# Performance work log

Measured on AMD Instinct MI355X. Metric: run time of the kernel, lower is better.

The kernel has to match this reference:

```python
import jax, jax.numpy as jnp
import numpy as np

D_MODEL = 1024
HEADS = 16
HEAD_DIM = D_MODEL // HEADS


def setup_inputs() -> dict:
    key = jax.random.key(0)
    ks = jax.random.split(key, 6)
    B, S, D = 2, 2048, D_MODEL
    scale = 1.0 / np.sqrt(D)
    x = jax.random.normal(ks[0], (B, S, D), dtype=jnp.float32)
    mask = jax.random.randint(ks[1], (B, S), 0, 2, dtype=jnp.int32)
    Wq = jax.random.normal(ks[2], (D, D), dtype=jnp.float32) * scale
    Wk = jax.random.normal(ks[3], (D, D), dtype=jnp.float32) * scale
    Wv = jax.random.normal(ks[4], (D, D), dtype=jnp.float32) * scale
    Wp = jax.random.normal(ks[5], (D, D), dtype=jnp.float32) * scale
    zb = jnp.zeros((D,), dtype=jnp.float32)
    return {"x": x, "mask": mask, "Wq": Wq, "bq": zb, "Wk": Wk, "bk": zb,
            "Wv": Wv, "bv": zb, "Wp": Wp, "bp": zb}


def reference(x, mask, Wq, bq, Wk, bk, Wv, bv, Wp, bp):
    B, S, D = x.shape
    H, Dh = HEADS, HEAD_DIM

    def split_heads(t):  # [B,S,D] -> [B,H,S,Dh]
        return t.reshape(B, S, H, Dh).transpose(0, 2, 1, 3)

    q = split_heads(x @ Wq + bq)
    k = split_heads(x @ Wk + bk)
    v = split_heads(x @ Wv + bv)

    att = jnp.einsum('bhqd,bhkd->bhqk', q, k) / jnp.sqrt(jnp.float32(Dh))
    # key-padding mask: [B,S] -> [B,1,1,S]; masked positions -> -inf
    m = (mask[:, None, None, :] != 0)
    att = jnp.where(m, att, -jnp.inf)
    att = jax.nn.softmax(att, axis=-1)
    # rows that were fully masked produce NaN -> zero them (masked_fill(isnan, 0))
    att = jnp.where(jnp.isnan(att), 0.0, att)

    y = jnp.einsum('bhqk,bhkd->bhqd', att, v)  # [B,H,S,Dh]
    y = y.transpose(0, 2, 1, 3).reshape(B, S, D)
    return y @ Wp + bp
```

## Files before the change

### kernel.cpp

```cpp
#include <hip/hip_runtime.h>
#include <math.h>

#define D_MODEL 1024
#define HEADS 16
#define HEAD_DIM 64
#define SEQ 2048
#define BATCH 2
#define KVT 64
#define QTILE 128
#define SCALE_Q 0.18033688f

typedef __attribute__((ext_vector_type(8))) short bf16x8;
typedef __attribute__((ext_vector_type(4))) float f32x4;

__device__ __forceinline__ short f2bf(float f) {
    union { float f; unsigned u; } v; v.f = f;
    unsigned r = (v.u + 0x7FFFu + ((v.u >> 16) & 1u)) >> 16;
    return (short)r;
}

__device__ __forceinline__ unsigned cvt_pk_bf16(float lo, float hi) {
    unsigned r;
    asm("v_cvt_pk_bf16_f32 %0, %1, %2" : "=v"(r) : "v"(lo), "v"(hi));
    return r;
}

__device__ __forceinline__ float fexp2(float x) {
    float r;
    asm("v_exp_f32 %0, %1" : "=v"(r) : "v"(x));
    return r;
}

__global__ __launch_bounds__(256) void prep(
    const float* __restrict__ x, const float* __restrict__ Wq,
    const float* __restrict__ Wk, const float* __restrict__ Wv,
    const float* __restrict__ Wp, const int* __restrict__ mask,
    short* __restrict__ xb, short* __restrict__ Wqkvt,
    short* __restrict__ Wpt, float* __restrict__ maskf) {
    __shared__ float t[32][33];
    const int bid = blockIdx.x;
    if (bid < 2048) {
        const int i = bid * 256 + threadIdx.x;
        float4 a = ((const float4*)x)[2 * i];
        float4 b = ((const float4*)x)[2 * i + 1];
        short r[8] = {f2bf(a.x), f2bf(a.y), f2bf(a.z), f2bf(a.w),
                      f2bf(b.x), f2bf(b.y), f2bf(b.z), f2bf(b.w)};
        *(uint4*)(xb + 8 * i) = *(uint4*)r;
    } else if (bid < 6144) {
        const int tt = bid - 2048;
        const int z = tt >> 10;
        const int rem = tt & 1023;
        const float* W = z == 0 ? Wq : z == 1 ? Wk : z == 2 ? Wv : Wp;
        short* dst = (z < 3) ? Wqkvt + (size_t)z * 1024 * 1024 : Wpt;
        const int n0 = (rem & 31) * 32, k0 = (rem >> 5) * 32;
        const int tx = threadIdx.x & 31, ty = threadIdx.x >> 5;
#pragma unroll
        for (int j = 0; j < 4; ++j)
            t[ty + j * 8][tx] = W[(size_t)(k0 + ty + j * 8) * 1024 + n0 + tx];
        __syncthreads();
#pragma unroll
        for (int j = 0; j < 4; ++j) {
            const int n = ty + j * 8;
            dst[(size_t)(n0 + n) * 1024 + k0 + tx] = f2bf(t[tx][n]);
        }
    } else {
        const int i = (bid - 6144) * 256 + threadIdx.x;
        maskf[i] = mask[i] ? 0.f : -INFINITY;
    }
}

template <int MODE>
__global__ __launch_bounds__(256) void mfma_gemm(
    const short* __restrict__ A, const short* __restrict__ Bt,
    const float* __restrict__ b0, const float* __restrict__ b1,
    const float* __restrict__ b2, float* __restrict__ outf,
    short* __restrict__ o0, short* __restrict__ o1, short* __restrict__ o2,
    int M, int N, int K) {
    __shared__ short As[2 * 128 * 32];
    __shared__ short Bs[2 * 128 * 32];

    const int tid = threadIdx.x;
    const int wave = tid >> 6, lane = tid & 63;
    const int l15 = lane & 15, lhi = lane >> 4;
    const int wm = wave >> 1, wn = wave & 1;

    const int nwgx = gridDim.x;
    const int nwg = nwgx * gridDim.y;
    const int lin = blockIdx.y * nwgx + blockIdx.x;
    const int swz = (lin & 7) * (nwg >> 3) + (lin >> 3);
    const int bm0 = (swz / nwgx) * 128, bn0 = (swz % nwgx) * 128;

    f32x4 acc[4][4];
#pragma unroll
    for (int m = 0; m < 4; ++m)
#pragma unroll
        for (int n = 0; n < 4; ++n) acc[m][n] = (f32x4){0.f, 0.f, 0.f, 0.f};

#define STAGE_G(buf, kt_)                                                         \
    {                                                                             \
        const int k0 = (kt_) * 32;                                                \
        _Pragma("unroll") for (int p = 0; p < 2; ++p) {                           \
            const int o = (wave * 2 + p) * 64 + lane;                             \
            const int r = o >> 2;                                                 \
            const int gs = (o & 3) ^ ((r >> 1) & 3);                              \
            __builtin_amdgcn_global_load_lds(                                     \
                (const __attribute__((address_space(1))) void*)(                  \
                    A + (size_t)(bm0 + r) * K + k0 + gs * 8),                     \
                (__attribute__((address_space(3))) void*)(                        \
                    As + (size_t)(buf) * 4096 + (wave * 2 + p) * 512),            \
                16, 0, 0);                                                        \
            __builtin_amdgcn_global_load_lds(                                     \
                (const __attribute__((address_space(1))) void*)(                  \
                    Bt + (size_t)(bn0 + r) * K + k0 + gs * 8),                    \
                (__attribute__((address_space(3))) void*)(                        \
                    Bs + (size_t)(buf) * 4096 + (wave * 2 + p) * 512),            \
                16, 0, 0);                                                        \
        }                                                                         \
    }

    const int NT = K / 32;
    STAGE_G(0, 0);
    __syncthreads();
    for (int kt = 0; kt < NT; ++kt) {
        const int cur = kt & 1;
        if (kt + 1 < NT) STAGE_G((kt + 1) & 1, kt + 1);
        bf16x8 af[4], bf[4];
        const int sg = (lhi ^ ((l15 >> 1) & 3)) * 16;
#pragma unroll
        for (int m = 0; m < 4; ++m)
            af[m] = *(const bf16x8*)((char*)As + cur * 8192 +
                                     (wm * 64 + m * 16 + l15) * 64 + sg);
#pragma unroll
        for (int n = 0; n < 4; ++n)
            bf[n] = *(const bf16x8*)((char*)Bs + cur * 8192 +
                                     (wn * 64 + n * 16 + l15) * 64 + sg);
        __builtin_amdgcn_s_setprio(1);
#pragma unroll
        for (int m = 0; m < 4; ++m)
#pragma unroll
            for (int n = 0; n < 4; ++n)
                acc[m][n] = __builtin_amdgcn_mfma_f32_16x16x32_bf16(af[m], bf[n], acc[m][n], 0, 0, 0);
        __builtin_amdgcn_s_setprio(0);
        __syncthreads();
    }
#undef STAGE_G

    const int which = (MODE == 1) ? (bn0 >> 10) : 0;
#pragma unroll
    for (int m = 0; m < 4; ++m) {
#pragma unroll
        for (int n = 0; n < 4; ++n) {
            const int col = bn0 + wn * 64 + n * 16 + l15;
            if (MODE == 0) {
#pragma unroll
                for (int rr = 0; rr < 4; ++rr) {
                    const int row = bm0 + wm * 64 + m * 16 + lhi * 4 + rr;
                    outf[(size_t)row * N + col] = acc[m][n][rr] + b0[col];
                }
            } else {
                const int cc = col & 1023;
                const int h = cc >> 6, dh = cc & 63;
                const int row0 = bm0 + wm * 64 + m * 16 + lhi * 4;
                const int b = row0 >> 11, s0 = row0 & (SEQ - 1);
                if (which == 2) {
                    const float bias = b2[cc];
                    uint2 w;
                    w.x = cvt_pk_bf16(acc[m][n][0] + bias, acc[m][n][1] + bias);
                    w.y = cvt_pk_bf16(acc[m][n][2] + bias, acc[m][n][3] + bias);
                    *(uint2*)(o2 + ((size_t)(b * HEADS + h) * HEAD_DIM + dh) * SEQ + s0) = w;
                } else {
                    const float bias = (which == 0 ? b0 : b1)[cc];
                    short* dst = which == 0 ? o0 : o1;
#pragma unroll
                    for (int rr = 0; rr < 4; ++rr) {
                        float v = acc[m][n][rr] + bias;
                        if (which == 0) v *= SCALE_Q;
                        dst[(((size_t)(b * HEADS + h)) * SEQ + s0 + rr) * HEAD_DIM + dh] = f2bf(v);
                    }
                }
            }
        }
    }
}

__global__ __launch_bounds__(256, 2) void flash_attn(
    const short* __restrict__ Q, const short* __restrict__ K,
    const short* __restrict__ Vt, const float* __restrict__ maskf,
    short* __restrict__ Y) {
    __shared__ unsigned char kt[2][KVT * 128];
    __shared__ unsigned char vt[2][HEAD_DIM * 128];
    __shared__ unsigned char pb[4][32 * 128];

    const int tid = threadIdx.x;
    const int wave = tid >> 6;
    const int lane = tid & 63;
    const int l15 = lane & 15;
    const int lhi = lane >> 4;

    const int nwg = gridDim.x;
    const int wg = blockIdx.x;
    const int swz = (wg & 7) * (nwg >> 3) + (wg >> 3);
    const int qt = swz & 15;
    const int bh = swz >> 4;
    const int b = bh >> 4;

    const int q0 = qt * QTILE + wave * 32;

    bf16x8 qf[2][2];
#pragma unroll
    for (int qi = 0; qi < 2; ++qi) {
        const short* Qp = Q + ((size_t)bh * SEQ + q0 + 16 * qi + l15) * HEAD_DIM;
        qf[qi][0] = *(const bf16x8*)(Qp + 8 * lhi);
        qf[qi][1] = *(const bf16x8*)(Qp + 8 * lhi + 32);
    }

    const unsigned char* Kb8 = (const unsigned char*)(K + (size_t)bh * SEQ * HEAD_DIM);
    const unsigned char* Vb8 = (const unsigned char*)(Vt + (size_t)bh * HEAD_DIM * SEQ);
    const float* mb = maskf + b * SEQ;

#define STAGE(buf, kvi)                                                            \
    {                                                                              \
        const unsigned char* kbase = Kb8 + (size_t)(kvi) * KVT * 128;              \
        const unsigned char* vbase = Vb8 + (size_t)(kvi) * 128;                    \
        _Pragma("unroll") for (int p = 0; p < 2; ++p) {                            \
            const int o = (wave * 2 + p) * 64 + lane;                              \
            const int row = o >> 3;                                                \
            const int inner = (o & 7) * 16;                                        \
            const int src = inner ^ ((row & 7) << 4);                              \
            __builtin_amdgcn_global_load_lds(                                      \
                (const __attribute__((address_space(1))) void*)(                   \
                    kbase + row * 128 + src),                                      \
                (__attribute__((address_space(3))) void*)(                         \
                    &kt[buf][(wave * 2 + p) * 1024]),                              \
                16, 0, 0);                                                         \
            __builtin_amdgcn_global_load_lds(                                      \
                (const __attribute__((address_space(1))) void*)(                   \
                    &vt[buf][0] == nullptr ? nullptr :                             \
                    vbase + (size_t)row * (SEQ * 2) + src),                        \
                (__attribute__((address_space(3))) void*)(                         \
                    &vt[buf][(wave * 2 + p) * 1024]),                              \
                16, 0, 0);                                                         \
        }                                                                          \
    }

    f32x4 accO[2][4];
    float lrow[2] = {0.f, 0.f};
#pragma unroll
    for (int qi = 0; qi < 2; ++qi)
#pragma unroll
        for (int i = 0; i < 4; ++i) accO[qi][i] = (f32x4){0.f, 0.f, 0.f, 0.f};

    STAGE(0, 0);
    asm volatile("s_waitcnt vmcnt(0)" ::: "memory");
    __builtin_amdgcn_s_barrier();

    for (int kv = 0; kv < SEQ / KVT; ++kv) {
        const int cur = kv & 1;
        if (kv + 1 < SEQ / KVT) STAGE((kv + 1) & 1, kv + 1);
        asm volatile("s_waitcnt vmcnt(4)" ::: "memory");
        __builtin_amdgcn_sched_barrier(0);
        __builtin_amdgcn_s_barrier();

        const int k0 = kv * KVT;

        f32x4 accS[2][4];
#pragma unroll
        for (int qi = 0; qi < 2; ++qi)
#pragma unroll
            for (int nt = 0; nt < 4; ++nt) accS[qi][nt] = (f32x4){0.f, 0.f, 0.f, 0.f};
#pragma unroll
        for (int c = 0; c < 2; ++c) {
            bf16x8 kf[4];
#pragma unroll
            for (int nt = 0; nt < 4; ++nt) {
                const int key = l15 + 16 * nt;
                kf[nt] = *(const bf16x8*)(kt[cur] + key * 128 +
                                          ((16 * lhi + 64 * c) ^ ((key & 7) << 4)));
            }
            __builtin_amdgcn_s_setprio(1);
#pragma unroll
            for (int qi = 0; qi < 2; ++qi)
#pragma unroll
                for (int nt = 0; nt < 4; ++nt)
                    accS[qi][nt] = __builtin_amdgcn_mfma_f32_16x16x32_bf16(
                        kf[nt], qf[qi][c], accS[qi][nt], 0, 0, 0);
            __builtin_amdgcn_s_setprio(0);
        }

        f32x4 ma[4];
#pragma unroll
        for (int nt = 0; nt < 4; ++nt)
            ma[nt] = *(const f32x4*)(mb + k0 + 16 * nt + 4 * lhi);

#pragma unroll
        for (int qi = 0; qi < 2; ++qi) {
#pragma unroll
            for (int nt = 0; nt < 4; ++nt) {
                f32x4 p;
#pragma unroll
                for (int r = 0; r < 4; ++r) {
                    p[r] = fexp2(accS[qi][nt][r] + ma[nt][r]);
                    lrow[qi] += p[r];
                }
                uint2 w;
                w.x = cvt_pk_bf16(p[0], p[1]);
                w.y = cvt_pk_bf16(p[2], p[3]);
                *(uint2*)(pb[wave] + (l15 + 16 * qi) * 128 +
                          ((32 * nt + 8 * lhi) ^ (l15 << 3))) = w;
            }
        }

#pragma unroll
        for (int c = 0; c < 2; ++c) {
            bf16x8 pf[2];
#pragma unroll
            for (int qi = 0; qi < 2; ++qi) {
                union { bf16x8 v; uint2 u[2]; } pfu;
                pfu.u[0] = *(const uint2*)(pb[wave] + (l15 + 16 * qi) * 128 +
                                           ((16 * lhi + 64 * c) ^ (l15 << 3)));
                pfu.u[1] = *(const uint2*)(pb[wave] + (l15 + 16 * qi) * 128 +
                                           ((16 * lhi + 64 * c + 8) ^ (l15 << 3)));
                pf[qi] = pfu.v;
            }
            bf16x8 vf[4];
#pragma unroll
            for (int d = 0; d < 4; ++d) {
                const int dh = l15 + 16 * d;
                vf[d] = *(const bf16x8*)(vt[cur] + dh * 128 +
                                         ((16 * lhi + 64 * c) ^ ((dh & 7) << 4)));
            }
            __builtin_amdgcn_s_setprio(1);
#pragma unroll
            for (int qi = 0; qi < 2; ++qi)
#pragma unroll
                for (int d = 0; d < 4; ++d)
                    accO[qi][d] = __builtin_amdgcn_mfma_f32_16x16x32_bf16(
                        vf[d], pf[qi], accO[qi][d], 0, 0, 0);
            __builtin_amdgcn_s_setprio(0);
        }
        __builtin_amdgcn_s_barrier();
    }
#undef STAGE

#pragma unroll
    for (int qi = 0; qi < 2; ++qi) {
        float rs = lrow[qi];
        rs += __shfl_xor(rs, 16);
        rs += __shfl_xor(rs, 32);
        const float inv = (rs > 0.f) ? 1.f / rs : 0.f;
        const int qg = q0 + 16 * qi + l15;
        short* Yp = Y + ((size_t)b * SEQ + qg) * D_MODEL + (bh & 15) * HEAD_DIM;
#pragma unroll
        for (int d = 0; d < 4; ++d) {
            uint2 w;
            w.x = cvt_pk_bf16(accO[qi][d][0] * inv, accO[qi][d][1] * inv);
            w.y = cvt_pk_bf16(accO[qi][d][2] * inv, accO[qi][d][3] * inv);
            *(uint2*)(Yp + 16 * d + 4 * lhi) = w;
        }
    }
}

extern "C" void kernel_launch(void* const* d_in, const int* in_sizes, int n_in,
                              void* d_out, int out_size, void* d_ws, size_t ws_size,
                              hipStream_t stream) {
    const float* x    = (const float*)d_in[0];
    const int*   mask = (const int*)  d_in[1];
    const float* Wq   = (const float*)d_in[2];
    const float* bq   = (const float*)d_in[3];
    const float* Wk   = (const float*)d_in[4];
    const float* bk   = (const float*)d_in[5];
    const float* Wv   = (const float*)d_in[6];
    const float* bv   = (const float*)d_in[7];
    const float* Wp   = (const float*)d_in[8];
    const float* bp   = (const float*)d_in[9];
    float* out = (float*)d_out;

    short* ws    = (short*)d_ws;
    short* xb    = ws;
    short* Wqkvt = xb + ((size_t)4 << 20);
    short* Wpt   = Wqkvt + ((size_t)3 << 20);
    short* Qb    = Wpt + ((size_t)1 << 20);
    short* Kb    = Qb + ((size_t)4 << 20);
    short* Vtb   = Kb + ((size_t)4 << 20);
    short* Yb    = Vtb + ((size_t)4 << 20);
    float* maskf = (float*)(Yb + ((size_t)4 << 20));

    const int M = BATCH * SEQ;

    prep<<<dim3(6160), 256, 0, stream>>>(x, Wq, Wk, Wv, Wp, mask,
                                         xb, Wqkvt, Wpt, maskf);

    mfma_gemm<1><<<dim3(3 * D_MODEL / 128, M / 128), 256, 0, stream>>>(
        xb, Wqkvt, bq, bk, bv, nullptr, Qb, Kb, Vtb, M, 3 * D_MODEL, D_MODEL);

    flash_attn<<<dim3(BATCH * HEADS * (SEQ / QTILE)), 256, 0, stream>>>(Qb, Kb, Vtb, maskf, Yb);

    mfma_gemm<0><<<dim3(D_MODEL / 128, M / 128), 256, 0, stream>>>(
        Yb, Wpt, bp, bp, bp, out, nullptr, nullptr, nullptr, M, D_MODEL, D_MODEL);
}
```

Before: 122.3 us.

## Software-pipeline QK^T one tile ahead of softmax/PV and stage mask in LDS

Restructures the flash-attention loop so the S=QK^T MFMAs for tile kv run in the same iteration as the exp/P·V work for tile kv-1, using ping-pong score accumulators and a triple-buffered V tile. This lets the matrix-core work overlap the transcendental and LDS softmax work within a wave. It also preloads the whole mask row into LDS at the start instead of reading it from global memory every tile. In exchange it uses more registers for two score accumulator sets and more LDS for the third V buffer and the 8 KB mask, which may lower occupancy.

```diff
diff --git a/kernel.cpp b/kernel.cpp
--- a/kernel.cpp
+++ b/kernel.cpp
@@ -188,8 +188,9 @@
     const short* __restrict__ Vt, const float* __restrict__ maskf,
     short* __restrict__ Y) {
     __shared__ unsigned char kt[2][KVT * 128];
-    __shared__ unsigned char vt[2][HEAD_DIM * 128];
+    __shared__ unsigned char vt[3][KVT * 128];
     __shared__ unsigned char pb[4][32 * 128];
+    __shared__ float mask_lds[SEQ];
 
     const int tid = threadIdx.x;
     const int wave = tid >> 6;
@@ -218,7 +219,7 @@
     const unsigned char* Vb8 = (const unsigned char*)(Vt + (size_t)bh * HEAD_DIM * SEQ);
     const float* mb = maskf + b * SEQ;
 
-#define STAGE(buf, kvi)                                                            \
+#define STAGE(kbuf, vbuf, kvi)                                                     \
     {                                                                              \
         const unsigned char* kbase = Kb8 + (size_t)(kvi) * KVT * 128;              \
         const unsigned char* vbase = Vb8 + (size_t)(kvi) * 128;                    \
@@ -231,67 +232,152 @@
                 (const __attribute__((address_space(1))) void*)(                   \
                     kbase + row * 128 + src),                                      \
                 (__attribute__((address_space(3))) void*)(                         \
-                    &kt[buf][(wave * 2 + p) * 1024]),                              \
+                    &kt[kbuf][(wave * 2 + p) * 1024]),                             \
                 16, 0, 0);                                                         \
             __builtin_amdgcn_global_load_lds(                                      \
                 (const __attribute__((address_space(1))) void*)(                   \
-                    &vt[buf][0] == nullptr ? nullptr :                             \
                     vbase + (size_t)row * (SEQ * 2) + src),                        \
                 (__attribute__((address_space(3))) void*)(                         \
-                    &vt[buf][(wave * 2 + p) * 1024]),                              \
+                    &vt[vbuf][(wave * 2 + p) * 1024]),                             \
                 16, 0, 0);                                                         \
         }                                                                          \
     }
 
-    f32x4 accO[2][4];
+    f32x4 accA[2][4], accB[2][4], accO[2][4];
     float lrow[2] = {0.f, 0.f};
 #pragma unroll
     for (int qi = 0; qi < 2; ++qi)
 #pragma unroll
         for (int i = 0; i < 4; ++i) accO[qi][i] = (f32x4){0.f, 0.f, 0.f, 0.f};
 
-    STAGE(0, 0);
+    {
+        const unsigned char* msrc = (const unsigned char*)mb;
+#pragma unroll
+        for (int p = 0; p < 2; ++p) {
+            __builtin_amdgcn_global_load_lds(
+                (const __attribute__((address_space(1))) void*)(
+                    msrc + ((wave * 2 + p) * 64 + lane) * 16),
+                (__attribute__((address_space(3))) void*)(
+                    (unsigned char*)mask_lds + (wave * 2 + p) * 1024),
+                16, 0, 0);
+        }
+    }
+    STAGE(0, 0, 0);
     asm volatile("s_waitcnt vmcnt(0)" ::: "memory");
+    __builtin_amdgcn_sched_barrier(0);
     __builtin_amdgcn_s_barrier();
-
-    for (int kv = 0; kv < SEQ / KVT; ++kv) {
-        const int cur = kv & 1;
-        if (kv + 1 < SEQ / KVT) STAGE((kv + 1) & 1, kv + 1);
-        asm volatile("s_waitcnt vmcnt(4)" ::: "memory");
-        __builtin_amdgcn_sched_barrier(0);
-        __builtin_amdgcn_s_barrier();
-
-        const int k0 = kv * KVT;
-
-        f32x4 accS[2][4];
+    STAGE(1, 1, 1);
+    {
+        const unsigned char* ktb = kt[0];
+        bf16x8 kf0[4], kf1[4];
+#pragma unroll
+        for (int nt = 0; nt < 4; ++nt) {
+            const int key = l15 + 16 * nt;
+            kf0[nt] = *(const bf16x8*)(ktb + key * 128 + ((16 * lhi) ^ ((key & 7) << 4)));
+            kf1[nt] = *(const bf16x8*)(ktb + key * 128 + ((16 * lhi + 64) ^ ((key & 7) << 4)));
+        }
 #pragma unroll
         for (int qi = 0; qi < 2; ++qi)
 #pragma unroll
-            for (int nt = 0; nt < 4; ++nt) accS[qi][nt] = (f32x4){0.f, 0.f, 0.f, 0.f};
-#pragma unroll
-        for (int c = 0; c < 2; ++c) {
-            bf16x8 kf[4];
-#pragma unroll
             for (int nt = 0; nt < 4; ++nt) {
-                const int key = l15 + 16 * nt;
-                kf[nt] = *(const bf16x8*)(kt[cur] + key * 128 +
-                                          ((16 * lhi + 64 * c) ^ ((key & 7) << 4)));
+                f32x4 t0 = __builtin_amdgcn_mfma_f32_16x16x32_bf16(
+                    kf0[nt], qf[qi][0], (f32x4){0.f, 0.f, 0.f, 0.f}, 0, 0, 0);
+                accA[qi][nt] = __builtin_amdgcn_mfma_f32_16x16x32_bf16(
+                    kf1[nt], qf[qi][1], t0, 0, 0, 0);
             }
-            __builtin_amdgcn_s_setprio(1);
-#pragma unroll
-            for (int qi = 0; qi < 2; ++qi)
-#pragma unroll
-                for (int nt = 0; nt < 4; ++nt)
-                    accS[qi][nt] = __builtin_amdgcn_mfma_f32_16x16x32_bf16(
-                        kf[nt], qf[qi][c], accS[qi][nt], 0, 0, 0);
-            __builtin_amdgcn_s_setprio(0);
-        }
-
+    }
+    __builtin_amdgcn_s_barrier();
+
+#define BODY(kv, CUR, PRV, DO_STAGE)                                               \
+    {                                                                              \
+        if (DO_STAGE) {                                                            \
+            STAGE(((kv) + 1) & 1, ((kv) + 1) % 3, (kv) + 1);                       \
+            asm volatile("s_waitcnt vmcnt(4)" ::: "memory");                       \
+        } else {                                                                   \
+            asm volatile("s_waitcnt vmcnt(0)" ::: "memory");                       \
+        }                                                                          \
+        __builtin_amdgcn_sched_barrier(0);                                         \
+        __builtin_amdgcn_s_barrier();                                              \
+        bf16x8 kf0[4], kf1[4];                                                     \
+        {                                                                          \
+            const unsigned char* ktb = kt[(kv) & 1];                               \
+            _Pragma("unroll") for (int nt = 0; nt < 4; ++nt) {                     \
+                const int key = l15 + 16 * nt;                                     \
+                kf0[nt] = *(const bf16x8*)(ktb + key * 128 +                       \
+                                           ((16 * lhi) ^ ((key & 7) << 4)));       \
+                kf1[nt] = *(const bf16x8*)(ktb + key * 128 +                       \
+                                           ((16 * lhi + 64) ^ ((key & 7) << 4)));  \
+            }                                                                      \
+        }                                                                          \
+                \
+        f32x4 ma[4];                                                               \
+        _Pragma("unroll") for (int nt = 0; nt < 4; ++nt)                           \
+            ma[nt] = *(const f32x4*)(&mask_lds[((kv) - 1) * 64 + 16 * nt + 4 * lhi]); \
+        _Pragma("unroll") for (int qi = 0; qi < 2; ++qi) {                         \
+            _Pragma("unroll") for (int nt = 0; nt < 4; ++nt) {                     \
+                f32x4 p;                                                           \
+                _Pragma("unroll") for (int r = 0; r < 4; ++r) {                    \
+                    p[r] = fexp2(PRV[qi][nt][r] + ma[nt][r]);                      \
+                    lrow[qi] += p[r];                                              \
+                }                                                                  \
+                uint2 w;                                                           \
+                w.x = cvt_pk_bf16(p[0], p[1]);                                     \
+                w.y = cvt_pk_bf16(p[2], p[3]);                                     \
+                *(uint2*)(pb[wave] + (l15 + 16 * qi) * 128 +                       \
+                          ((32 * nt + 8 * lhi) ^ (l15 << 3))) = w;                 \
+            }                                                                      \
+        }                                                                          \
+                            \
+        __builtin_amdgcn_s_setprio(1);                                             \
+        _Pragma("unroll") for (int qi = 0; qi < 2; ++qi)                           \
+            _Pragma("unroll") for (int nt = 0; nt < 4; ++nt) {                     \
+                f32x4 t0 = __builtin_amdgcn_mfma_f32_16x16x32_bf16(                \
+                    kf0[nt], qf[qi][0], (f32x4){0.f, 0.f, 0.f, 0.f}, 0, 0, 0);     \
+                CUR[qi][nt] = __builtin_amdgcn_mfma_f32_16x16x32_bf16(             \
+                    kf1[nt], qf[qi][1], t0, 0, 0, 0);                              \
+            }                                                                      \
+        __builtin_amdgcn_s_setprio(0);                                             \
+                                                             \
+        {                                                                          \
+            const unsigned char* vtb = vt[((kv) - 1) % 3];                         \
+            _Pragma("unroll") for (int c = 0; c < 2; ++c) {                        \
+                bf16x8 pf[2];                                                      \
+                _Pragma("unroll") for (int qi = 0; qi < 2; ++qi) {                 \
+                    union { bf16x8 v; uint2 u[2]; } pfu;                           \
+                    pfu.u[0] = *(const uint2*)(pb[wave] + (l15 + 16 * qi) * 128 +  \
+                                               ((16 * lhi + 64 * c) ^ (l15 << 3))); \
+                    pfu.u[1] = *(const uint2*)(pb[wave] + (l15 + 16 * qi) * 128 +  \
+                                               ((16 * lhi + 64 * c + 8) ^ (l15 << 3))); \
+                    pf[qi] = pfu.v;                                                \
+                }                                                                  \
+                bf16x8 vf[4];                                                      \
+                _Pragma("unroll") for (int d = 0; d < 4; ++d) {                    \
+                    const int dh = l15 + 16 * d;                                   \
+                    vf[d] = *(const bf16x8*)(vtb + dh * 128 +                      \
+                                             ((16 * lhi + 64 * c) ^ ((dh & 7) << 4))); \
+                }                                                                  \
+                __builtin_amdgcn_s_setprio(1);                                     \
+                _Pragma("unroll") for (int qi = 0; qi < 2; ++qi)                   \
+                    _Pragma("unroll") for (int d = 0; d < 4; ++d)                  \
+                        accO[qi][d] = __builtin_amdgcn_mfma_f32_16x16x32_bf16(     \
+                            vf[d], pf[qi], accO[qi][d], 0, 0, 0);                  \
+                __builtin_amdgcn_s_setprio(0);                                     \
+            }                                                                      \
+        }                                                                          \
+        __builtin_amdgcn_s_barrier();                                              \
+    }
+
+    for (int kv = 1; kv <= 29; kv += 2) {
+        BODY(kv, accB, accA, 1);
+        BODY(kv + 1, accA, accB, 1);
+    }
+    BODY(31, accB, accA, 0);
+
+    {
         f32x4 ma[4];
 #pragma unroll
         for (int nt = 0; nt < 4; ++nt)
-            ma[nt] = *(const f32x4*)(mb + k0 + 16 * nt + 4 * lhi);
-
+            ma[nt] = *(const f32x4*)(&mask_lds[31 * 64 + 16 * nt + 4 * lhi]);
 #pragma unroll
         for (int qi = 0; qi < 2; ++qi) {
 #pragma unroll
@@ -299,7 +385,7 @@
                 f32x4 p;
 #pragma unroll
                 for (int r = 0; r < 4; ++r) {
-                    p[r] = fexp2(accS[qi][nt][r] + ma[nt][r]);
+                    p[r] = fexp2(accB[qi][nt][r] + ma[nt][r]);
                     lrow[qi] += p[r];
                 }
                 uint2 w;
@@ -309,7 +395,7 @@
                           ((32 * nt + 8 * lhi) ^ (l15 << 3))) = w;
             }
         }
-
+        const unsigned char* vtb = vt[31 % 3];
 #pragma unroll
         for (int c = 0; c < 2; ++c) {
             bf16x8 pf[2];
@@ -326,20 +412,18 @@
 #pragma unroll
             for (int d = 0; d < 4; ++d) {
                 const int dh = l15 + 16 * d;
-                vf[d] = *(const bf16x8*)(vt[cur] + dh * 128 +
+                vf[d] = *(const bf16x8*)(vtb + dh * 128 +
                                          ((16 * lhi + 64 * c) ^ ((dh & 7) << 4)));
             }
-            __builtin_amdgcn_s_setprio(1);
 #pragma unroll
             for (int qi = 0; qi < 2; ++qi)
 #pragma unroll
                 for (int d = 0; d < 4; ++d)
                     accO[qi][d] = __builtin_amdgcn_mfma_f32_16x16x32_bf16(
                         vf[d], pf[qi], accO[qi][d], 0, 0, 0);
-            __builtin_amdgcn_s_setprio(0);
-        }
-        __builtin_amdgcn_s_barrier();
-    }
+        }
+    }
+#undef BODY
 #undef STAGE
 
 #pragma unroll
```

Result: faster. 119.1 us, median of 2 (-2.6%).
